# Performance work log

Hardware: AMD Instinct MI355X
Metric: run time of the kernel (lower is better)

The kernel has to match this reference:

```python
import jax, jax.numpy as jnp
import numpy as np

B, T, D_MODEL, H, RPR_K = 2, 2048, 1024, 16, 8
DK = D_MODEL // H  # 64
NUM_RPR = 2 * RPR_K + 1


def setup_inputs() -> dict:
    key = jax.random.key(0)
    ks = jax.random.split(key, 16)
    s = 0.02
    inp = {
        "query": jax.random.normal(ks[0], (B, T, D_MODEL), jnp.float32),
        "key": jax.random.normal(ks[1], (B, T, D_MODEL), jnp.float32),
        "value": jax.random.normal(ks[2], (B, T, D_MODEL), jnp.float32),
        "mask": jnp.ones((B, 1, 1, T), dtype=bool),
        "w_q": jax.random.normal(ks[3], (D_MODEL, H * DK), jnp.float32) * s,
        "b_q": jnp.zeros((H * DK,), jnp.float32),
        "w_k": jax.random.normal(ks[4], (D_MODEL, H * DK), jnp.float32) * s,
        "b_k": jnp.zeros((H * DK,), jnp.float32),
        "w_v": jax.random.normal(ks[5], (D_MODEL, H * DK), jnp.float32) * s,
        "b_v": jnp.zeros((H * DK,), jnp.float32),
        "w_o": jax.random.normal(ks[6], (H * DK, D_MODEL), jnp.float32) * s,
        "b_o": jnp.zeros((D_MODEL,), jnp.float32),
        "rpr_key_table": jax.random.normal(ks[7], (NUM_RPR, DK), jnp.float32),
        "rpr_value_table": jax.random.normal(ks[8], (NUM_RPR, DK), jnp.float32),
    }
    return inp


def _rel_edges(seq_len):
    # edges[i, j] = clamp(j - i + rpr_k, 0, 2*rpr_k)  -> [T, T] int32
    seq = jnp.arange(seq_len)
    edges = seq[None, :] - seq[:, None] + RPR_K
    return jnp.clip(edges, 0, 2 * RPR_K)


def reference(query, key, value, mask, w_q, b_q, w_k, b_k, w_v, b_v,
              w_o, b_o, rpr_key_table, rpr_value_table):
    Bsz, Tlen, _ = query.shape
    edges = _rel_edges(Tlen)                       # [T, T]
    ek = rpr_key_table[edges]                      # [T, T, DK]
    ev = rpr_value_table[edges]                    # [T, T, DK]

    def proj(x, w, b):
        return (x @ w + b).reshape(Bsz, Tlen, H, DK).transpose(0, 2, 1, 3)  # [B,H,T,DK]

    q = proj(query, w_q, b_q)
    k = proj(key, w_k, b_k)
    v = proj(value, w_v, b_v)

    scores_qk = jnp.einsum('bhtd,bhsd->bhts', q, k)
    scores_qek = jnp.einsum('bhtd,tsd->bhts', q, ek)
    scores = (scores_qk + scores_qek) / jnp.sqrt(jnp.float32(DK))
    scores = jnp.where(mask, scores, jnp.float32(-1e9))
    a = jax.nn.softmax(scores, axis=-1)            # [B,H,T,T]

    upd = jnp.einsum('bhts,bhsd->bhtd', a, v)
    upd_e = jnp.einsum('bhts,tsd->bhtd', a, ev)
    x = (upd + upd_e).transpose(0, 2, 1, 3).reshape(Bsz, Tlen, H * DK)
    return x @ w_o + b_o
```

## Files before the change

### kernel.cpp

```cpp
#include <hip/hip_runtime.h>
#include <stdint.h>


typedef unsigned short u16;
typedef __attribute__((ext_vector_type(4))) float f32x4;
typedef __attribute__((ext_vector_type(4))) int   i32x4;
typedef __attribute__((ext_vector_type(8))) __bf16 bh8;

#define T_LEN 2048
#define NHEAD 16
#define NR    17

#define SCALE_LOG2 0.18033688011112042f
#define CLAMP_LOG2 86.56170245333781f

__device__ __forceinline__ float bf2f(u16 x) {
  unsigned u = ((unsigned)x) << 16;
  return __builtin_bit_cast(float, u);
}
__device__ __forceinline__ u16 f2bf(float f) {
  unsigned u = __builtin_bit_cast(unsigned, f);
  u = u + 0x7fffu + ((u >> 16) & 1u);
  return (u16)(u >> 16);
}
__device__ __forceinline__ f32x4 zero4() { f32x4 z = {0.f, 0.f, 0.f, 0.f}; return z; }

__device__ __forceinline__ f32x4 mfma16(bh8 a, bh8 b, f32x4 c) {
  return __builtin_amdgcn_mfma_f32_16x16x32_bf16(a, b, c, 0, 0, 0);
}

__device__ __forceinline__ void bar_sync() {
  __builtin_amdgcn_sched_barrier(0);
  asm volatile("s_waitcnt lgkmcnt(0)" ::: "memory");
  __builtin_amdgcn_s_barrier();
  __builtin_amdgcn_sched_barrier(0);
}

__device__ __forceinline__ void async16(const u16* g, u16* l) {
  __builtin_amdgcn_global_load_lds(
      (const __attribute__((address_space(1))) void*)g,
      (__attribute__((address_space(3))) void*)l, 16, 0, 0);
}

__device__ __forceinline__ bh8 ldfrag(const u16* base, int row, int qc) {
  const i32x4 v = *(const i32x4*)(base + row * 64 + ((qc ^ (row & 7)) << 3));
  return __builtin_bit_cast(bh8, v);
}

__global__ __launch_bounds__(256) void prep_kernel(
    const float* __restrict__ xq, const float* __restrict__ xk,
    const float* __restrict__ xv, const float* __restrict__ w0,
    const float* __restrict__ w1, const float* __restrict__ w2,
    const float* __restrict__ w3, u16* __restrict__ oq, u16* __restrict__ ok,
    u16* __restrict__ ov, u16* __restrict__ t0, u16* __restrict__ t1,
    u16* __restrict__ t2, u16* __restrict__ t3) {
  __shared__ u16 tile[32][33];
  const int z = blockIdx.z;
  if (z < 3) {
    const float* S = (z == 0) ? xq : (z == 1) ? xk : xv;
    u16* D = (z == 0) ? oq : (z == 1) ? ok : ov;
    const size_t i = ((size_t)blockIdx.x * 256 + threadIdx.x) * 8;
    const f32x4 v0 = *(const f32x4*)(S + i);
    const f32x4 v1 = *(const f32x4*)(S + i + 4);
    u16 o[8];
#pragma unroll
    for (int j = 0; j < 4; ++j) {
      o[j] = f2bf(v0[j]);
      o[4 + j] = f2bf(v1[j]);
    }
    i32x4 w;
    __builtin_memcpy(&w, o, 16);
    *(i32x4*)(D + i) = w;
  } else {
    if (blockIdx.x >= 1024) return;
    const float* S = (z == 3) ? w0 : (z == 4) ? w1 : (z == 5) ? w2 : w3;
    u16* D = (z == 3) ? t0 : (z == 4) ? t1 : (z == 5) ? t2 : t3;
    const int tx = threadIdx.x & 31, ty = threadIdx.x >> 5;
    const int bx = blockIdx.x & 31, by = blockIdx.x >> 5;
#pragma unroll
    for (int i = 0; i < 4; ++i) {
      const int y = by * 32 + ty + i * 8;
      tile[ty + i * 8][tx] = f2bf(S[(size_t)y * 1024 + bx * 32 + tx]);
    }
    __syncthreads();
#pragma unroll
    for (int i = 0; i < 4; ++i) {
      const int y = bx * 32 + ty + i * 8;
      D[(size_t)y * 1024 + by * 32 + tx] = tile[tx][ty + i * 8];
    }
  }
}

__device__ __forceinline__ void gemm_body(const u16* __restrict__ A,
                                          const u16* __restrict__ Bm,
                                          const float* __restrict__ bias,
                                          void* __restrict__ out, int mode,
                                          int bm, int bn) {
  __shared__ __align__(16) u16 As[2][128 * 32];
  __shared__ __align__(16) u16 Bs[2][128 * 32];
  const int tid = threadIdx.x;
  const int wv = tid >> 6;
  const int ln = tid & 63;
  const int quad = ln >> 4, l15 = ln & 15;
  const int wr = wv >> 1, wc = wv & 1;

  f32x4 acc[4][4];
#pragma unroll
  for (int i = 0; i < 4; ++i)
#pragma unroll
    for (int j = 0; j < 4; ++j) acc[i][j] = zero4();

  const int c0 = tid, c1 = tid + 256;
  const size_t aoff0 = (size_t)(bm * 128 + (c0 >> 2)) * 1024 + (c0 & 3) * 8;
  const size_t aoff1 = (size_t)(bm * 128 + (c1 >> 2)) * 1024 + (c1 & 3) * 8;
  const size_t boff0 = (size_t)(bn * 128 + (c0 >> 2)) * 1024 + (c0 & 3) * 8;
  const size_t boff1 = (size_t)(bn * 128 + (c1 >> 2)) * 1024 + (c1 & 3) * 8;

  u16* ad0[2] = {&As[0][(wv * 64) * 8], &As[1][(wv * 64) * 8]};
  u16* ad1[2] = {&As[0][(256 + wv * 64) * 8], &As[1][(256 + wv * 64) * 8]};
  u16* bd0[2] = {&Bs[0][(wv * 64) * 8], &Bs[1][(wv * 64) * 8]};
  u16* bd1[2] = {&Bs[0][(256 + wv * 64) * 8], &Bs[1][(256 + wv * 64) * 8]};

  async16(A + aoff0, ad0[0]);
  async16(A + aoff1, ad1[0]);
  async16(Bm + boff0, bd0[0]);
  async16(Bm + boff1, bd1[0]);
  __syncthreads();

  for (int kt = 0; kt < 32; ++kt) {
    const int cur = kt & 1, nxt = cur ^ 1;
    if (kt < 31) {
      const int ko = (kt + 1) * 32;
      async16(A + aoff0 + ko, ad0[nxt]);
      async16(A + aoff1 + ko, ad1[nxt]);
      async16(Bm + boff0 + ko, bd0[nxt]);
      async16(Bm + boff1 + ko, bd1[nxt]);
    }

    bh8 af[4], bf[4];
#pragma unroll
    for (int mi = 0; mi < 4; ++mi)
      af[mi] = __builtin_bit_cast(
          bh8,
          *(const i32x4*)&As[cur][(wr * 64 + mi * 16 + l15) * 32 + quad * 8]);
#pragma unroll
    for (int ni = 0; ni < 4; ++ni)
      bf[ni] = __builtin_bit_cast(
          bh8,
          *(const i32x4*)&Bs[cur][(wc * 64 + ni * 16 + l15) * 32 + quad * 8]);
#pragma unroll
    for (int mi = 0; mi < 4; ++mi)
#pragma unroll
      for (int ni = 0; ni < 4; ++ni)
        acc[mi][ni] = mfma16(af[mi], bf[ni], acc[mi][ni]);

    __syncthreads();
  }

#pragma unroll
  for (int mi = 0; mi < 4; ++mi) {
    const int row0 = bm * 128 + wr * 64 + mi * 16 + quad * 4;
#pragma unroll
    for (int ni = 0; ni < 4; ++ni) {
      const int col = bn * 128 + wc * 64 + ni * 16 + l15;
      const float bcol = (mode == 3) ? 0.f : bias[col];
#pragma unroll
      for (int reg = 0; reg < 4; ++reg) {
        const int r = row0 + reg;
        const float v = acc[mi][ni][reg] + ((mode == 3) ? bias[r] : bcol);
        if (mode == 0) {
          ((float*)out)[(size_t)r * 1024 + col] = v;
        } else if (mode == 1) {
          const int bb = r >> 11, t = r & 2047;
          const int h = col >> 6, d = col & 63;
          ((u16*)out)[(((size_t)bb * NHEAD + h) * T_LEN + (size_t)t) * 64 + d] =
              f2bf(v);
        } else {
          const int h = r >> 6, d = r & 63;
          const int bb = col >> 11, t = col & 2047;
          ((u16*)out)[(((size_t)bb * NHEAD + h) * 64 + (size_t)d) * T_LEN + t] =
              f2bf(v);
        }
      }
    }
  }
}

__global__ __launch_bounds__(256) void gemm_qkv_kernel(
    const u16* __restrict__ xq, const u16* __restrict__ xk,
    const u16* __restrict__ xv, const u16* __restrict__ wtq,
    const u16* __restrict__ wtk, const u16* __restrict__ wtv,
    const float* __restrict__ bq, const float* __restrict__ bk,
    const float* __restrict__ bv, u16* __restrict__ oq, u16* __restrict__ ok,
    u16* __restrict__ ovt) {
  const int z = blockIdx.z;
  if (z == 0)
    gemm_body(xq, wtq, bq, oq, 1, blockIdx.x, blockIdx.y);
  else if (z == 1)
    gemm_body(xk, wtk, bk, ok, 1, blockIdx.x, blockIdx.y);
  else
    gemm_body(wtv, xv, bv, ovt, 3, blockIdx.y, blockIdx.x);
}

__global__ __launch_bounds__(256) void gemm_o_kernel(const u16* __restrict__ X,
                                                     const u16* __restrict__ Wt,
                                                     const float* __restrict__ bias,
                                                     float* __restrict__ out) {
  gemm_body(X, Wt, bias, out, 0, blockIdx.x, blockIdx.y);
}

__global__ __launch_bounds__(512) void attn_kernel(
    const u16* __restrict__ Qw, const u16* __restrict__ Kw,
    const u16* __restrict__ Vtw, const float* __restrict__ rkt,
    const float* __restrict__ rvt, u16* __restrict__ U) {
  __shared__ __align__(16) u16 smu[12288];
  __shared__ float smf[3648];
  u16* Qs = smu;
  u16* Ps = smu;
  u16* Ks = smu + 4096;
  u16* Vs = smu + 8192;
  float* qes = smf;
  float* aw = smf + 1088;
  float* rvs = smf + 2176;
  float* lp = smf + 3264;
  float* s0p = smf + 3392;
  float* s16p = smf + 3520;
  float* osum = (float*)smu;

  const int tid = threadIdx.x;
  const int wv = tid >> 6, ln = tid & 63;
  const int tg = wv & 3, sh = wv >> 2;
  const int quad = ln >> 4, l15 = ln & 15;
  const int qt = blockIdx.x, bh = blockIdx.y;
  const size_t hb = (size_t)bh * (T_LEN * 64);

  {
    const int row = tid >> 3, gc = tid & 7;
    i32x4 v = *(const i32x4*)&Qw[hb + (size_t)(qt * 64 + row) * 64 + gc * 8];
    *(i32x4*)&Qs[row * 64 + ((gc ^ (row & 7)) << 3)] = v;
  }
  __syncthreads();

  for (int i = tid; i < 64 * NR; i += 512) {
    const int row = i / NR, r = i - row * NR;
    float s = 0.f;
#pragma unroll
    for (int c = 0; c < 8; ++c) {
      const i32x4 qv = *(const i32x4*)&Qs[row * 64 + ((c ^ (row & 7)) << 3)];
      const u16* qq = (const u16*)&qv;
#pragma unroll
      for (int j = 0; j < 8; ++j) s += bf2f(qq[j]) * rkt[r * 64 + c * 8 + j];
    }
    qes[i] = s;
    aw[i] = 0.f;
  }
  for (int i = tid; i < NR * 64; i += 512) rvs[i] = rvt[i];
  __syncthreads();

  const int myrow = tg * 16 + l15;
  const bh8 qf0 = ldfrag(Qs, myrow, quad);
  const bh8 qf1 = ldfrag(Qs, myrow, quad + 4);
  const float qb0 = qes[myrow * NR + 0] * SCALE_LOG2;
  const float qb16 = qes[myrow * NR + 16] * SCALE_LOG2;

  float l_lane = 0.f, s0_lane = 0.f, s16_lane = 0.f;
  f32x4 oacc[4];
#pragma unroll
  for (int r = 0; r < 4; ++r) oacc[r] = zero4();

  const int kr = tid >> 3, kg = tid & 7;
  const int kls = kr * 64 + ((kg ^ (kr & 7)) << 3);

  i32x4 kp = *(const i32x4*)&Kw[hb + (size_t)kr * 64 + kg * 8];
  i32x4 vp = *(const i32x4*)&Vtw[hb + (size_t)kr * T_LEN + kg * 8];

  for (int st = 0; st < 32; ++st) {
    *(i32x4*)&Ks[kls] = kp;
    *(i32x4*)&Vs[kls] = vp;
    if (st < 31) {
      kp = *(const i32x4*)&Kw[hb + (size_t)((st + 1) * 64 + kr) * 64 + kg * 8];
      vp = *(const i32x4*)&Vtw[hb + (size_t)kr * T_LEN + (st + 1) * 64 + kg * 8];
    }
    bar_sync();

    __builtin_amdgcn_s_setprio(1);
    f32x4 sacc[2];
#pragma unroll
    for (int m2 = 0; m2 < 2; ++m2) {
      const int mi = sh * 2 + m2;
      bh8 kf0 = ldfrag(Ks, mi * 16 + l15, quad);
      bh8 kf1 = ldfrag(Ks, mi * 16 + l15, quad + 4);
      sacc[m2] = mfma16(kf0, qf0, zero4());
      sacc[m2] = mfma16(kf1, qf1, sacc[m2]);
    }

    float p[2][4];
    const bool band = (st >= qt - 1) && (st <= qt + 1);
    if (!band) {
      const bool lo = (st < qt);
      const float qb = lo ? qb0 : qb16;
      float ts = 0.f;
#pragma unroll
      for (int m2 = 0; m2 < 2; ++m2)
#pragma unroll
        for (int reg = 0; reg < 4; ++reg) {
          const float x = fminf(sacc[m2][reg] * SCALE_LOG2 + qb, CLAMP_LOG2);
          const float pv = __builtin_amdgcn_exp2f(x);
          p[m2][reg] = pv;
          ts += pv;
        }
      l_lane += ts;
      if (lo)
        s0_lane += ts;
      else
        s16_lane += ts;
    } else {
      const int tgl = qt * 64 + myrow;
#pragma unroll
      for (int m2 = 0; m2 < 2; ++m2)
#pragma unroll
        for (int reg = 0; reg < 4; ++reg) {
          const int sg = st * 64 + (sh * 2 + m2) * 16 + quad * 4 + reg;
          int rel = sg - tgl + 8;
          rel = rel < 0 ? 0 : (rel > 16 ? 16 : rel);
          const float x =
              fminf((sacc[m2][reg] + qes[myrow * NR + rel]) * SCALE_LOG2,
                    CLAMP_LOG2);
          const float pv = __builtin_amdgcn_exp2f(x);
          p[m2][reg] = pv;
          l_lane += pv;
          if (rel == 0)
            s0_lane += pv;
          else if (rel == 16)
            s16_lane += pv;
          else
            atomicAdd(&aw[myrow * NR + rel], pv);
        }
    }

#pragma unroll
    for (int m2 = 0; m2 < 2; ++m2) {
      const unsigned long long w =
          (unsigned long long)f2bf(p[m2][0]) |
          ((unsigned long long)f2bf(p[m2][1]) << 16) |
          ((unsigned long long)f2bf(p[m2][2]) << 32) |
          ((unsigned long long)f2bf(p[m2][3]) << 48);
      const int qc = 2 * (sh * 2 + m2) + (quad >> 1);
      *(unsigned long long*)&Ps[myrow * 64 + ((qc ^ (myrow & 7)) << 3) +
                                (quad & 1) * 4] = w;
    }

    {
      const int qc = sh * 4 + quad;
      const bh8 pf = ldfrag(Ps, myrow, qc);
#pragma unroll
      for (int ni = 0; ni < 4; ++ni) {
        bh8 vf = ldfrag(Vs, ni * 16 + l15, qc);
        oacc[ni] = mfma16(pf, vf, oacc[ni]);
      }
    }
    __builtin_amdgcn_s_setprio(0);
    bar_sync();
  }

  l_lane += __shfl_xor(l_lane, 16);
  l_lane += __shfl_xor(l_lane, 32);
  s0_lane += __shfl_xor(s0_lane, 16);
  s0_lane += __shfl_xor(s0_lane, 32);
  s16_lane += __shfl_xor(s16_lane, 16);
  s16_lane += __shfl_xor(s16_lane, 32);
  if (quad == 0) {
    lp[sh * 64 + myrow] = l_lane;
    s0p[sh * 64 + myrow] = s0_lane;
    s16p[sh * 64 + myrow] = s16_lane;
  }
  {
    const int oni0 = (1 - sh) * 2;
#pragma unroll
    for (int m2 = 0; m2 < 2; ++m2)
#pragma unroll
      for (int reg = 0; reg < 4; ++reg)
        osum[(tg * 16 + quad * 4 + reg) * 65 + (oni0 + m2) * 16 + l15] =
            oacc[oni0 + m2][reg];
  }
  __syncthreads();

  for (int i = tid; i < 64 * NR; i += 512) {
    const int row = i / NR, rr = i - row * NR;
    float v = aw[i];
    if (rr == 0) v += s0p[row] + s0p[64 + row];
    if (rr == 16) v += s16p[row] + s16p[64 + row];
    aw[i] = v;
  }
  if (tid < 64) lp[tid] += lp[64 + tid];
  __syncthreads();

  const int bb = bh >> 4, hh = bh & 15;
  const int trow = tg * 16 + quad * 4;
#pragma unroll
  for (int m2 = 0; m2 < 2; ++m2) {
    const int nip = sh * 2 + m2;
    const int d = nip * 16 + l15;
#pragma unroll
    for (int reg = 0; reg < 4; ++reg) {
      const int rowi = trow + reg;
      float o = oacc[nip][reg] + osum[rowi * 65 + d];
      float e = 0.f;
#pragma unroll
      for (int rr = 0; rr < NR; ++rr)
        e += aw[rowi * NR + rr] * rvs[rr * 64 + d];
      const float ov = (o + e) / lp[rowi];
      const int tgl = qt * 64 + rowi;
      U[((size_t)bb * T_LEN + tgl) * 1024 + hh * 64 + d] = f2bf(ov);
    }
  }
}

extern "C" void kernel_launch(void* const* d_in, const int* in_sizes, int n_in,
                              void* d_out, int out_size, void* d_ws,
                              size_t ws_size, hipStream_t stream) {
  const float* query = (const float*)d_in[0];
  const float* key = (const float*)d_in[1];
  const float* value = (const float*)d_in[2];
  const float* w_q = (const float*)d_in[4];
  const float* b_q = (const float*)d_in[5];
  const float* w_k = (const float*)d_in[6];
  const float* b_k = (const float*)d_in[7];
  const float* w_v = (const float*)d_in[8];
  const float* b_v = (const float*)d_in[9];
  const float* w_o = (const float*)d_in[10];
  const float* b_o = (const float*)d_in[11];
  const float* rkt = (const float*)d_in[12];
  const float* rvt = (const float*)d_in[13];

  char* ws = (char*)d_ws;
  const size_t MB2 = 1u << 21, MB8 = 1u << 23;
  u16* wtq = (u16*)(ws + 0 * MB2);
  u16* wtk = (u16*)(ws + 1 * MB2);
  u16* wtv = (u16*)(ws + 2 * MB2);
  u16* wto = (u16*)(ws + 3 * MB2);
  u16* Xq = (u16*)(ws + 4 * MB2 + 0 * MB8);
  u16* Xk = (u16*)(ws + 4 * MB2 + 1 * MB8);
  u16* Xv = (u16*)(ws + 4 * MB2 + 2 * MB8);
  u16* Qw = (u16*)(ws + 4 * MB2 + 3 * MB8);
  u16* Kw = (u16*)(ws + 4 * MB2 + 4 * MB8);
  u16* Vtw = (u16*)(ws + 4 * MB2 + 5 * MB8);
  u16* Uw = (u16*)(ws + 4 * MB2 + 6 * MB8);

  prep_kernel<<<dim3(2048, 1, 7), 256, 0, stream>>>(
      query, key, value, w_q, w_k, w_v, w_o, Xq, Xk, Xv, wtq, wtk, wtv, wto);
  gemm_qkv_kernel<<<dim3(32, 8, 3), 256, 0, stream>>>(
      Xq, Xk, Xv, wtq, wtk, wtv, b_q, b_k, b_v, Qw, Kw, Vtw);
  attn_kernel<<<dim3(32, 32), 512, 0, stream>>>(Qw, Kw, Vtw, rkt, rvt, Uw);
  gemm_o_kernel<<<dim3(32, 8), 256, 0, stream>>>(Uw, wto, b_o, (float*)d_out);
}
```

Baseline: 333.8 us.

## Double-buffer K/V tiles in LDS via async global-to-LDS loads

Replaces the register-staged K/V prefetch with global_load_lds direct-to-LDS copies into two ping-pong buffers. Q is also loaded the same way, with the XOR swizzle applied on the source side. The per-iteration barrier count drops from two to one, and the register round trip through VGPRs is removed. The rel-value table staging moves to the epilogue so its LDS space can be reused, at the cost of more LDS per block, which may reduce occupancy.

New measurement: 366.6 us. 1.1x slower.

```diff
diff --git a/kernel.cpp b/kernel.cpp
--- a/kernel.cpp
+++ b/kernel.cpp
@@ -33,6 +33,12 @@
   __builtin_amdgcn_sched_barrier(0);
   asm volatile("s_waitcnt lgkmcnt(0)" ::: "memory");
   __builtin_amdgcn_s_barrier();
+  __builtin_amdgcn_sched_barrier(0);
+}
+
+__device__ __forceinline__ void wait_vm0() {
+  __builtin_amdgcn_sched_barrier(0);
+  asm volatile("s_waitcnt vmcnt(0)" ::: "memory");
   __builtin_amdgcn_sched_barrier(0);
 }
 
@@ -213,19 +219,17 @@
     const u16* __restrict__ Qw, const u16* __restrict__ Kw,
     const u16* __restrict__ Vtw, const float* __restrict__ rkt,
     const float* __restrict__ rvt, u16* __restrict__ U) {
-  __shared__ __align__(16) u16 smu[12288];
-  __shared__ float smf[3648];
+  __shared__ __align__(16) u16 smu[20480];
+  __shared__ float smf[2560];
   u16* Qs = smu;
   u16* Ps = smu;
-  u16* Ks = smu + 4096;
-  u16* Vs = smu + 8192;
   float* qes = smf;
   float* aw = smf + 1088;
-  float* rvs = smf + 2176;
-  float* lp = smf + 3264;
-  float* s0p = smf + 3392;
-  float* s16p = smf + 3520;
+  float* lp = smf + 2176;
+  float* s0p = smf + 2304;
+  float* s16p = smf + 2432;
   float* osum = (float*)smu;
+  float* rvs = (float*)(smu + 12288);
 
   const int tid = threadIdx.x;
   const int wv = tid >> 6, ln = tid & 63;
@@ -234,12 +238,20 @@
   const int qt = blockIdx.x, bh = blockIdx.y;
   const size_t hb = (size_t)bh * (T_LEN * 64);
 
-  {
-    const int row = tid >> 3, gc = tid & 7;
-    i32x4 v = *(const i32x4*)&Qw[hb + (size_t)(qt * 64 + row) * 64 + gc * 8];
-    *(i32x4*)&Qs[row * 64 + ((gc ^ (row & 7)) << 3)] = v;
-  }
-  __syncthreads();
+  const int kr = tid >> 3;
+  const int kgp = (tid & 7) ^ ((tid >> 3) & 7);
+  const u16* qsrc = Qw + hb + (size_t)(qt * 64 + kr) * 64 + kgp * 8;
+  const u16* ksrc = Kw + hb + (size_t)kr * 64 + kgp * 8;
+  const u16* vsrc = Vtw + hb + (size_t)kr * T_LEN + kgp * 8;
+  u16* const ldsQ = smu + wv * 512;
+  u16* const ldsK0 = smu + 4096 + wv * 512;
+  u16* const ldsV0 = smu + 12288 + wv * 512;
+
+  async16(qsrc, ldsQ);
+  async16(ksrc, ldsK0);
+  async16(vsrc, ldsV0);
+  wait_vm0();
+  bar_sync();
 
   for (int i = tid; i < 64 * NR; i += 512) {
     const int row = i / NR, r = i - row * NR;
@@ -254,12 +266,13 @@
     qes[i] = s;
     aw[i] = 0.f;
   }
-  for (int i = tid; i < NR * 64; i += 512) rvs[i] = rvt[i];
-  __syncthreads();
 
   const int myrow = tg * 16 + l15;
   const bh8 qf0 = ldfrag(Qs, myrow, quad);
   const bh8 qf1 = ldfrag(Qs, myrow, quad + 4);
+
+  bar_sync();
+
   const float qb0 = qes[myrow * NR + 0] * SCALE_LOG2;
   const float qb16 = qes[myrow * NR + 16] * SCALE_LOG2;
 
@@ -268,28 +281,23 @@
 #pragma unroll
   for (int r = 0; r < 4; ++r) oacc[r] = zero4();
 
-  const int kr = tid >> 3, kg = tid & 7;
-  const int kls = kr * 64 + ((kg ^ (kr & 7)) << 3);
-
-  i32x4 kp = *(const i32x4*)&Kw[hb + (size_t)kr * 64 + kg * 8];
-  i32x4 vp = *(const i32x4*)&Vtw[hb + (size_t)kr * T_LEN + kg * 8];
-
   for (int st = 0; st < 32; ++st) {
-    *(i32x4*)&Ks[kls] = kp;
-    *(i32x4*)&Vs[kls] = vp;
+    const int cur = st & 1;
+    const u16* Kc = smu + 4096 + cur * 4096;
+    const u16* Vc = smu + 12288 + cur * 4096;
     if (st < 31) {
-      kp = *(const i32x4*)&Kw[hb + (size_t)((st + 1) * 64 + kr) * 64 + kg * 8];
-      vp = *(const i32x4*)&Vtw[hb + (size_t)kr * T_LEN + (st + 1) * 64 + kg * 8];
-    }
-    bar_sync();
+      const int nxt = cur ^ 1;
+      async16(ksrc + (size_t)(st + 1) * 4096, ldsK0 + nxt * 4096);
+      async16(vsrc + (size_t)(st + 1) * 64, ldsV0 + nxt * 4096);
+    }
 
     __builtin_amdgcn_s_setprio(1);
     f32x4 sacc[2];
 #pragma unroll
     for (int m2 = 0; m2 < 2; ++m2) {
       const int mi = sh * 2 + m2;
-      bh8 kf0 = ldfrag(Ks, mi * 16 + l15, quad);
-      bh8 kf1 = ldfrag(Ks, mi * 16 + l15, quad + 4);
+      bh8 kf0 = ldfrag(Kc, mi * 16 + l15, quad);
+      bh8 kf1 = ldfrag(Kc, mi * 16 + l15, quad + 4);
       sacc[m2] = mfma16(kf0, qf0, zero4());
       sacc[m2] = mfma16(kf1, qf1, sacc[m2]);
     }
@@ -355,11 +363,13 @@
       const bh8 pf = ldfrag(Ps, myrow, qc);
 #pragma unroll
       for (int ni = 0; ni < 4; ++ni) {
-        bh8 vf = ldfrag(Vs, ni * 16 + l15, qc);
+        bh8 vf = ldfrag(Vc, ni * 16 + l15, qc);
         oacc[ni] = mfma16(pf, vf, oacc[ni]);
       }
     }
     __builtin_amdgcn_s_setprio(0);
+
+    wait_vm0();
     bar_sync();
   }
 
@@ -383,6 +393,7 @@
         osum[(tg * 16 + quad * 4 + reg) * 65 + (oni0 + m2) * 16 + l15] =
             oacc[oni0 + m2][reg];
   }
+  for (int i = tid; i < NR * 64; i += 512) rvs[i] = rvt[i];
   __syncthreads();
 
   for (int i = tid; i < 64 * NR; i += 512) {
```
